# Performance work log

Measured on AMD Instinct MI355X. Metric: run time of the kernel, lower is better.

The kernel has to match this reference:

```python
import jax, jax.numpy as jnp
import numpy as np

H = 2048      # hidden_size
I = 8192      # dense intermediate_size
MI = 1024     # moe_intermediate_size
E = 8         # num_local_experts
K = 2         # num_experts_per_tok
B, S = 2, 1024
EPS = 1e-6
ROOT = H ** (-0.5)


def _rms(x, w=None, eps=EPS):
    # fp32 RMSNorm matching _Gemma4CPURMSNorm; w=None -> no-scale variant
    ms = jnp.mean(x * x, axis=-1, keepdims=True) + eps
    y = x * jax.lax.rsqrt(ms)
    return y * w if w is not None else y


def _gelu_tanh(x):
    # gelu_pytorch_tanh == tanh-approximate gelu
    return jax.nn.gelu(x, approximate=True)


def setup_inputs() -> dict:
    key = jax.random.key(0)
    ks = jax.random.split(key, 10)
    s = 0.02
    return {
        "hidden_states": jax.random.normal(ks[0], (B, S, H), jnp.float32),
        # RMSNorm scales (init ones, as in nn.Parameter(torch.ones(dim)))
        "rn_pre1": jnp.ones((H,), jnp.float32),
        "rn_pre2": jnp.ones((H,), jnp.float32),
        "rn_post1": jnp.ones((H,), jnp.float32),
        "rn_post2": jnp.ones((H,), jnp.float32),
        "rn_post": jnp.ones((H,), jnp.float32),
        # dense GLU MLP weights, stored (in, out)
        "w_gate": jax.random.normal(ks[1], (H, I), jnp.float32) * s,
        "w_up":   jax.random.normal(ks[2], (H, I), jnp.float32) * s,
        "w_down": jax.random.normal(ks[3], (I, H), jnp.float32) * s,
        # router
        "router_w": jax.random.normal(ks[4], (H, E), jnp.float32) * s,
        "router_scale": jnp.ones((H,), jnp.float32),
        "per_expert_scale": jnp.ones((E,), jnp.float32),
        # per-expert GLU weights, stacked over experts
        "we_gate": jax.random.normal(ks[5], (E, H, MI), jnp.float32) * s,
        "we_up":   jax.random.normal(ks[6], (E, H, MI), jnp.float32) * s,
        "we_down": jax.random.normal(ks[7], (E, MI, H), jnp.float32) * s,
    }


def reference(hidden_states, rn_pre1, rn_pre2, rn_post1, rn_post2, rn_post,
              w_gate, w_up, w_down, router_w, router_scale, per_expert_scale,
              we_gate, we_up, we_down):
    b, s, h = hidden_states.shape
    T = b * s

    # --- dense branch ---
    dense_in = _rms(hidden_states, rn_pre1)                      # (B,S,H)
    dense_out = (_gelu_tanh(dense_in @ w_gate) * (dense_in @ w_up)) @ w_down
    dense_out = _rms(dense_out, rn_post1)                        # (B,S,H)

    # --- router (takes the raw residual, applies its own no-scale RMSNorm) ---
    x = hidden_states.reshape(T, h)
    xr = _rms(x) * router_scale * ROOT                           # (T,H)
    router_logits = xr @ router_w                                # (T,E)
    probs = jax.nn.softmax(router_logits, axis=-1)
    top_w, top_i = jax.lax.top_k(probs, K)                       # (T,K)
    top_w = top_w / jnp.sum(top_w, axis=-1, keepdims=True)
    top_w = top_w * per_expert_scale[top_i]
    aff = jnp.zeros((T, E), x.dtype).at[jnp.arange(T)[:, None], top_i].set(top_w)

    # --- MoE experts (compute all experts, combine with sparse affinities) ---
    moe_in = _rms(hidden_states, rn_pre2).reshape(T, h)          # (T,H)
    g = jnp.einsum('th,ehm->tem', moe_in, we_gate)               # (T,E,MI)
    u = jnp.einsum('th,ehm->tem', moe_in, we_up)
    eo = jnp.einsum('tem,emh->teh', _gelu_tanh(g) * u, we_down)  # (T,E,H)
    moe_out = jnp.einsum('te,teh->th', aff, eo).reshape(b, s, h)
    moe_out = _rms(moe_out, rn_post2)

    return _rms(dense_out + moe_out, rn_post)
```

## Files before the change

kernel.cpp:

```cpp
#include <hip/hip_runtime.h>
#include <stdint.h>

#define TOK 2048
#define HD  2048
#define ID  8192
#define MID 1024
#define NE  8
#define KSPLIT 4

typedef __attribute__((ext_vector_type(8))) short s16x8;
typedef __attribute__((ext_vector_type(4))) short s16x4;
typedef __attribute__((ext_vector_type(4))) float f32x4;

constexpr float EPSF  = 1e-6f;
constexpr float ROOTF = 0.02209708691207961f;

#define MFMA(a, b, c) __builtin_amdgcn_mfma_f32_16x16x32_bf16(a, b, c, 0, 0, 0)

__device__ __forceinline__ void gload16(const void* g, void* l) {
  __builtin_amdgcn_global_load_lds(
      (const __attribute__((address_space(1))) void*)g,
      (__attribute__((address_space(3))) void*)l, 16, 0, 0);
}

__device__ __forceinline__ short f2bf(float f) {
  union { float f; uint32_t u; } v; v.f = f;
  uint32_t r = v.u + 0x7fffu + ((v.u >> 16) & 1u);
  return (short)(r >> 16);
}

__device__ __forceinline__ float gelu_tanh(float x) {
  float x3 = x * x * x;
  float u = 0.7978845608028654f * (x + 0.044715f * x3);
  return 0.5f * x * (1.0f + tanhf(u));
}

__global__ __launch_bounds__(256) void k_rms_router(
    const float* __restrict__ x, const float* __restrict__ rnp1,
    const float* __restrict__ rnp2, const float* __restrict__ rsc,
    const float* __restrict__ rw, const float* __restrict__ pes,
    short* __restrict__ rms1, short* __restrict__ rms2,
    int* __restrict__ cnt, int* __restrict__ tokl,
    float* __restrict__ wgtl, int* __restrict__ slotl) {
  const int t = blockIdx.x, tid = threadIdx.x;
  const size_t base = (size_t)t * HD;
  f32x4 v[2];
  float ss = 0.f;
#pragma unroll
  for (int i = 0; i < 2; ++i) {
    v[i] = *(const f32x4*)(x + base + tid * 4 + i * 1024);
#pragma unroll
    for (int j = 0; j < 4; ++j) ss += v[i][j] * v[i][j];
  }
  __shared__ float sr[4];
  __shared__ float sl[32];
#pragma unroll
  for (int off = 32; off; off >>= 1) ss += __shfl_down(ss, off, 64);
  if ((tid & 63) == 0) sr[tid >> 6] = ss;
  __syncthreads();
  const float inv = rsqrtf((sr[0] + sr[1] + sr[2] + sr[3]) * (1.0f / HD) + EPSF);
  float p[8] = {0, 0, 0, 0, 0, 0, 0, 0};
#pragma unroll
  for (int i = 0; i < 2; ++i) {
    const int h = tid * 4 + i * 1024;
    f32x4 w1 = *(const f32x4*)(rnp1 + h);
    f32x4 w2 = *(const f32x4*)(rnp2 + h);
    f32x4 sc = *(const f32x4*)(rsc + h);
    s16x4 o1, o2;
#pragma unroll
    for (int j = 0; j < 4; ++j) {
      float xn = v[i][j] * inv;
      o1[j] = f2bf(xn * w1[j]);
      o2[j] = f2bf(xn * w2[j]);
      float xq = xn * sc[j] * ROOTF;
      const float* rr = rw + (size_t)(h + j) * NE;
      f32x4 ra = *(const f32x4*)rr;
      f32x4 rb = *(const f32x4*)(rr + 4);
      p[0] += xq * ra[0]; p[1] += xq * ra[1]; p[2] += xq * ra[2]; p[3] += xq * ra[3];
      p[4] += xq * rb[0]; p[5] += xq * rb[1]; p[6] += xq * rb[2]; p[7] += xq * rb[3];
    }
    *(s16x4*)(rms1 + base + h) = o1;
    *(s16x4*)(rms2 + base + h) = o2;
  }
#pragma unroll
  for (int e = 0; e < 8; ++e)
#pragma unroll
    for (int off = 32; off; off >>= 1) p[e] += __shfl_down(p[e], off, 64);
  if ((tid & 63) == 0) {
#pragma unroll
    for (int e = 0; e < 8; ++e) sl[(tid >> 6) * 8 + e] = p[e];
  }
  __syncthreads();
  if (tid == 0) {
    float l[8];
#pragma unroll
    for (int e = 0; e < 8; ++e) l[e] = sl[e] + sl[8 + e] + sl[16 + e] + sl[24 + e];
    int i1 = 0;
#pragma unroll
    for (int e = 1; e < 8; ++e) if (l[e] > l[i1]) i1 = e;
    int i2 = (i1 == 0) ? 1 : 0;
#pragma unroll
    for (int e = 0; e < 8; ++e) if (e != i1 && l[e] > l[i2]) i2 = e;
    float p2 = expf(l[i2] - l[i1]);
    float s = 1.0f + p2;
    float w1 = (1.0f / s) * pes[i1];
    float w2 = (p2 / s) * pes[i2];
    int q1 = atomicAdd(&cnt[i1], 1);
    tokl[i1 * TOK + q1] = t; wgtl[i1 * TOK + q1] = w1; slotl[i1 * TOK + q1] = 0;
    int q2 = atomicAdd(&cnt[i2], 1);
    tokl[i2 * TOK + q2] = t; wgtl[i2 * TOK + q2] = w2; slotl[i2 * TOK + q2] = 1;
  }
}

__global__ __launch_bounds__(256) void k_transpose(
    const float* __restrict__ in, short* __restrict__ out, int R, int C) {
  __shared__ float tile[64 * 65];
  const int tid = threadIdx.x;
  const int c0 = blockIdx.x * 64, r0 = blockIdx.y * 64;
  const size_t bo = (size_t)blockIdx.z * R * C;
#pragma unroll
  for (int i = 0; i < 4; ++i) {
    int idx = tid + 256 * i;
    int r = idx >> 4, c4 = idx & 15;
    f32x4 f = *(const f32x4*)(in + bo + (size_t)(r0 + r) * C + c0 + c4 * 4);
#pragma unroll
    for (int j = 0; j < 4; ++j) tile[(c4 * 4 + j) * 65 + r] = f[j];
  }
  __syncthreads();
#pragma unroll
  for (int i = 0; i < 2; ++i) {
    int ch = tid + 256 * i;
    int c = ch >> 3, rs = ch & 7;
    s16x8 o;
#pragma unroll
    for (int q = 0; q < 8; ++q) o[q] = f2bf(tile[c * 65 + rs * 8 + q]);
    *(s16x8*)(out + bo + (size_t)(c0 + c) * R + r0 + rs * 8) = o;
  }
}

__global__ __launch_bounds__(256) void k_dense_gateup(
    const short* __restrict__ wgT, const short* __restrict__ wuT,
    const short* __restrict__ xin,
    short* __restrict__ act) {
  __shared__ short sW[128 * 32];
  __shared__ short sX[128 * 32];
  const int tid = threadIdx.x;
  const int n0 = blockIdx.x * 64, t0 = blockIdx.y * 128;
  const int lane = tid & 63, wave = tid >> 6;
  const int ln15 = lane & 15, k8 = (lane >> 4) * 8;
  const int nsub = (wave & 1) * 32, tsub = (wave >> 1) * 64;
  const int srow = tid >> 2, skc = (tid & 3) * 8;
  const short* gW0 = wgT + (size_t)(n0 + srow) * HD + skc;
  const short* gW1 = wuT + (size_t)(n0 + srow) * HD + skc;
  const short* gX0 = xin + (size_t)(t0 + srow) * HD + skc;
  const short* gX1 = xin + (size_t)(t0 + 64 + srow) * HD + skc;
  char* lW = (char*)sW + wave * 1024;
  char* lX = (char*)sX + wave * 1024;
  f32x4 accg[2][4], accu[2][4];
#pragma unroll
  for (int m = 0; m < 2; ++m)
#pragma unroll
    for (int n = 0; n < 4; ++n) { accg[m][n] = (f32x4)0.f; accu[m][n] = (f32x4)0.f; }
  for (int kt = 0; kt < HD / 32; ++kt) {
    const int ko = kt * 32;
    __syncthreads();
    gload16(gW0 + ko, lW);
    gload16(gW1 + ko, lW + 4096);
    gload16(gX0 + ko, lX);
    gload16(gX1 + ko, lX + 4096);
    __syncthreads();
    s16x8 ag[2], au[2], bx[4];
#pragma unroll
    for (int m = 0; m < 2; ++m) {
      ag[m] = *(const s16x8*)(sW + (nsub + m * 16 + ln15) * 32 + k8);
      au[m] = *(const s16x8*)(sW + (64 + nsub + m * 16 + ln15) * 32 + k8);
    }
#pragma unroll
    for (int n = 0; n < 4; ++n)
      bx[n] = *(const s16x8*)(sX + (tsub + n * 16 + ln15) * 32 + k8);
#pragma unroll
    for (int m = 0; m < 2; ++m)
#pragma unroll
      for (int n = 0; n < 4; ++n) {
        accg[m][n] = MFMA(ag[m], bx[n], accg[m][n]);
        accu[m][n] = MFMA(au[m], bx[n], accu[m][n]);
      }
  }
#pragma unroll
  for (int m = 0; m < 2; ++m)
#pragma unroll
    for (int n = 0; n < 4; ++n) {
      const int t = t0 + tsub + n * 16 + ln15;
      const int ib = n0 + nsub + m * 16 + (lane >> 4) * 4;
      s16x4 o;
#pragma unroll
      for (int r = 0; r < 4; ++r)
        o[r] = f2bf(gelu_tanh(accg[m][n][r]) * accu[m][n][r]);
      *(s16x4*)(act + (size_t)t * ID + ib) = o;
    }
}

__global__ __launch_bounds__(256) void k_dense_down(
    const short* __restrict__ wdT,
    const short* __restrict__ act,
    float* __restrict__ dparts) {
  __shared__ short sW[128 * 32];
  __shared__ short sX[128 * 32];
  const int tid = threadIdx.x;
  const int n0 = blockIdx.x * 128, t0 = blockIdx.y * 128;
  const int kbase = blockIdx.z * (ID / KSPLIT);
  const int lane = tid & 63, wave = tid >> 6;
  const int wr = wave >> 1, wc = wave & 1;
  const int ln15 = lane & 15, k8 = (lane >> 4) * 8;
  const int srow = tid >> 2, skc = (tid & 3) * 8;
  const short* gW0 = wdT + (size_t)(n0 + srow) * ID + kbase + skc;
  const short* gW1 = wdT + (size_t)(n0 + 64 + srow) * ID + kbase + skc;
  const short* gX0 = act + (size_t)(t0 + srow) * ID + kbase + skc;
  const short* gX1 = act + (size_t)(t0 + 64 + srow) * ID + kbase + skc;
  char* lW = (char*)sW + wave * 1024;
  char* lX = (char*)sX + wave * 1024;
  f32x4 acc[4][4];
#pragma unroll
  for (int m = 0; m < 4; ++m)
#pragma unroll
    for (int n = 0; n < 4; ++n) acc[m][n] = (f32x4)0.f;
  for (int kt = 0; kt < ID / KSPLIT / 32; ++kt) {
    const int ko = kt * 32;
    __syncthreads();
    gload16(gW0 + ko, lW);
    gload16(gW1 + ko, lW + 4096);
    gload16(gX0 + ko, lX);
    gload16(gX1 + ko, lX + 4096);
    __syncthreads();
    s16x8 a[4], b[4];
#pragma unroll
    for (int m = 0; m < 4; ++m)
      a[m] = *(const s16x8*)(sW + (wr * 64 + m * 16 + ln15) * 32 + k8);
#pragma unroll
    for (int n = 0; n < 4; ++n)
      b[n] = *(const s16x8*)(sX + (wc * 64 + n * 16 + ln15) * 32 + k8);
#pragma unroll
    for (int m = 0; m < 4; ++m)
#pragma unroll
      for (int n = 0; n < 4; ++n) acc[m][n] = MFMA(a[m], b[n], acc[m][n]);
  }
  float* dst = dparts + (size_t)blockIdx.z * TOK * HD;
#pragma unroll
  for (int n = 0; n < 4; ++n) {
    const int t = t0 + wc * 64 + n * 16 + ln15;
#pragma unroll
    for (int m = 0; m < 4; ++m) {
      const int h = n0 + wr * 64 + m * 16 + (lane >> 4) * 4;
      *(f32x4*)(dst + (size_t)t * HD + h) = acc[m][n];
    }
  }
}

__global__ __launch_bounds__(256) void k_exp_gateup(
    const short* __restrict__ wegT, const short* __restrict__ weuT,
    const short* __restrict__ rms2,
    const int* __restrict__ cnt, const int* __restrict__ tokl,
    short* __restrict__ acte) {
  const int e = blockIdx.z;
  const int cn = cnt[e];
  const int t0 = blockIdx.y * 128;
  if (t0 >= cn) return;
  const int n0 = blockIdx.x * 64;
  __shared__ short sW[128 * 32];
  __shared__ short sX[128 * 32];
  const int tid = threadIdx.x;
  const int lane = tid & 63, wave = tid >> 6;
  const int ln15 = lane & 15, k8 = (lane >> 4) * 8;
  const int nsub = (wave & 1) * 32, tsub = (wave >> 1) * 64;
  const int srow = tid >> 2, skc = (tid & 3) * 8;
  const int* tl = tokl + e * TOK;
  int r0 = t0 + srow, r1 = t0 + 64 + srow;
  int tk0 = tl[r0 < cn ? r0 : cn - 1];
  int tk1 = tl[r1 < cn ? r1 : cn - 1];
  const short* gW0 = wegT + (size_t)e * MID * HD + (size_t)(n0 + srow) * HD + skc;
  const short* gW1 = weuT + (size_t)e * MID * HD + (size_t)(n0 + srow) * HD + skc;
  const short* gX0 = rms2 + (size_t)tk0 * HD + skc;
  const short* gX1 = rms2 + (size_t)tk1 * HD + skc;
  char* lW = (char*)sW + wave * 1024;
  char* lX = (char*)sX + wave * 1024;
  f32x4 accg[2][4], accu[2][4];
#pragma unroll
  for (int m = 0; m < 2; ++m)
#pragma unroll
    for (int n = 0; n < 4; ++n) { accg[m][n] = (f32x4)0.f; accu[m][n] = (f32x4)0.f; }
  for (int kt = 0; kt < HD / 32; ++kt) {
    const int ko = kt * 32;
    __syncthreads();
    gload16(gW0 + ko, lW);
    gload16(gW1 + ko, lW + 4096);
    gload16(gX0 + ko, lX);
    gload16(gX1 + ko, lX + 4096);
    __syncthreads();
    s16x8 ag[2], au[2], bx[4];
#pragma unroll
    for (int m = 0; m < 2; ++m) {
      ag[m] = *(const s16x8*)(sW + (nsub + m * 16 + ln15) * 32 + k8);
      au[m] = *(const s16x8*)(sW + (64 + nsub + m * 16 + ln15) * 32 + k8);
    }
#pragma unroll
    for (int n = 0; n < 4; ++n)
      bx[n] = *(const s16x8*)(sX + (tsub + n * 16 + ln15) * 32 + k8);
#pragma unroll
    for (int m = 0; m < 2; ++m)
#pragma unroll
      for (int n = 0; n < 4; ++n) {
        accg[m][n] = MFMA(ag[m], bx[n], accg[m][n]);
        accu[m][n] = MFMA(au[m], bx[n], accu[m][n]);
      }
  }
#pragma unroll
  for (int m = 0; m < 2; ++m)
#pragma unroll
    for (int n = 0; n < 4; ++n) {
      const int r = t0 + tsub + n * 16 + ln15;
      if (r < cn) {
        const int ib = n0 + nsub + m * 16 + (lane >> 4) * 4;
        s16x4 o;
#pragma unroll
        for (int q = 0; q < 4; ++q)
          o[q] = f2bf(gelu_tanh(accg[m][n][q]) * accu[m][n][q]);
        *(s16x4*)(acte + (size_t)e * TOK * MID + (size_t)r * MID + ib) = o;
      }
    }
}

__global__ __launch_bounds__(256) void k_exp_down(
    const short* __restrict__ wedT,
    const short* __restrict__ acte,
    const int* __restrict__ cnt, const int* __restrict__ tokl,
    const float* __restrict__ wgtl, const int* __restrict__ slotl,
    float* __restrict__ moep) {
  const int e = blockIdx.z;
  const int cn = cnt[e];
  const int t0 = blockIdx.y * 128;
  if (t0 >= cn) return;
  const int n0 = blockIdx.x * 128;
  __shared__ short sW[128 * 32];
  __shared__ short sX[128 * 32];
  const int tid = threadIdx.x;
  const int lane = tid & 63, wave = tid >> 6;
  const int wr = wave >> 1, wc = wave & 1;
  const int ln15 = lane & 15, k8 = (lane >> 4) * 8;
  const int srow = tid >> 2, skc = (tid & 3) * 8;
  const short* wb = wedT + (size_t)e * HD * MID;
  const short* gW0 = wb + (size_t)(n0 + srow) * MID + skc;
  const short* gW1 = wb + (size_t)(n0 + 64 + srow) * MID + skc;
  const short* ab = acte + (size_t)e * TOK * MID;
  const short* gX0 = ab + (size_t)(t0 + srow) * MID + skc;
  const short* gX1 = ab + (size_t)(t0 + 64 + srow) * MID + skc;
  char* lW = (char*)sW + wave * 1024;
  char* lX = (char*)sX + wave * 1024;
  f32x4 acc[4][4];
#pragma unroll
  for (int m = 0; m < 4; ++m)
#pragma unroll
    for (int n = 0; n < 4; ++n) acc[m][n] = (f32x4)0.f;
  for (int kt = 0; kt < MID / 32; ++kt) {
    const int ko = kt * 32;
    __syncthreads();
    gload16(gW0 + ko, lW);
    gload16(gW1 + ko, lW + 4096);
    gload16(gX0 + ko, lX);
    gload16(gX1 + ko, lX + 4096);
    __syncthreads();
    s16x8 a[4], b[4];
#pragma unroll
    for (int m = 0; m < 4; ++m)
      a[m] = *(const s16x8*)(sW + (wr * 64 + m * 16 + ln15) * 32 + k8);
#pragma unroll
    for (int n = 0; n < 4; ++n)
      b[n] = *(const s16x8*)(sX + (wc * 64 + n * 16 + ln15) * 32 + k8);
#pragma unroll
    for (int m = 0; m < 4; ++m)
#pragma unroll
      for (int n = 0; n < 4; ++n) acc[m][n] = MFMA(a[m], b[n], acc[m][n]);
  }
#pragma unroll
  for (int n = 0; n < 4; ++n) {
    const int r = t0 + wc * 64 + n * 16 + ln15;
    if (r < cn) {
      const int tk = tokl[e * TOK + r];
      const float wf = wgtl[e * TOK + r];
      const int sl = slotl[e * TOK + r];
      float* dst = moep + (size_t)sl * TOK * HD + (size_t)tk * HD;
#pragma unroll
      for (int m = 0; m < 4; ++m) {
        const int h = n0 + wr * 64 + m * 16 + (lane >> 4) * 4;
        f32x4 v = acc[m][n] * wf;
        *(f32x4*)(dst + h) = v;
      }
    }
  }
}

__global__ __launch_bounds__(256) void k_final(
    const float* __restrict__ dparts, const float* __restrict__ moep,
    const float* __restrict__ rno1, const float* __restrict__ rno2,
    const float* __restrict__ rnof, float* __restrict__ out) {
  const int t = blockIdx.x, tid = threadIdx.x;
  const size_t base = (size_t)t * HD;
  f32x4 dv[2], mv[2];
  float ssd = 0.f, ssm = 0.f;
#pragma unroll
  for (int i = 0; i < 2; ++i) {
    const int h = tid * 4 + i * 1024;
    dv[i] = (f32x4)0.f;
#pragma unroll
    for (int z = 0; z < KSPLIT; ++z)
      dv[i] += *(const f32x4*)(dparts + (size_t)z * TOK * HD + base + h);
    f32x4 a = *(const f32x4*)(moep + base + h);
    f32x4 b = *(const f32x4*)(moep + (size_t)TOK * HD + base + h);
    mv[i] = a + b;
#pragma unroll
    for (int j = 0; j < 4; ++j) { ssd += dv[i][j] * dv[i][j]; ssm += mv[i][j] * mv[i][j]; }
  }
  __shared__ float sr[8];
#pragma unroll
  for (int off = 32; off; off >>= 1) {
    ssd += __shfl_down(ssd, off, 64);
    ssm += __shfl_down(ssm, off, 64);
  }
  if ((tid & 63) == 0) { sr[tid >> 6] = ssd; sr[4 + (tid >> 6)] = ssm; }
  __syncthreads();
  const float invd = rsqrtf((sr[0] + sr[1] + sr[2] + sr[3]) * (1.0f / HD) + EPSF);
  const float invm = rsqrtf((sr[4] + sr[5] + sr[6] + sr[7]) * (1.0f / HD) + EPSF);
  f32x4 y[2];
  float ssy = 0.f;
#pragma unroll
  for (int i = 0; i < 2; ++i) {
    const int h = tid * 4 + i * 1024;
    f32x4 w1 = *(const f32x4*)(rno1 + h);
    f32x4 w2 = *(const f32x4*)(rno2 + h);
#pragma unroll
    for (int j = 0; j < 4; ++j) {
      y[i][j] = dv[i][j] * invd * w1[j] + mv[i][j] * invm * w2[j];
      ssy += y[i][j] * y[i][j];
    }
  }
  __syncthreads();
#pragma unroll
  for (int off = 32; off; off >>= 1) ssy += __shfl_down(ssy, off, 64);
  if ((tid & 63) == 0) sr[tid >> 6] = ssy;
  __syncthreads();
  const float invy = rsqrtf((sr[0] + sr[1] + sr[2] + sr[3]) * (1.0f / HD) + EPSF);
#pragma unroll
  for (int i = 0; i < 2; ++i) {
    const int h = tid * 4 + i * 1024;
    f32x4 w = *(const f32x4*)(rnof + h);
    f32x4 o;
#pragma unroll
    for (int j = 0; j < 4; ++j) o[j] = y[i][j] * invy * w[j];
    *(f32x4*)(out + base + h) = o;
  }
}

extern "C" void kernel_launch(void* const* d_in, const int* in_sizes, int n_in,
                              void* d_out, int out_size, void* d_ws, size_t ws_size,
                              hipStream_t stream) {
  (void)in_sizes; (void)n_in; (void)out_size;
  const float* x    = (const float*)d_in[0];
  const float* rnp1 = (const float*)d_in[1];
  const float* rnp2 = (const float*)d_in[2];
  const float* rno1 = (const float*)d_in[3];
  const float* rno2 = (const float*)d_in[4];
  const float* rnof = (const float*)d_in[5];
  const float* wg   = (const float*)d_in[6];
  const float* wu   = (const float*)d_in[7];
  const float* wd   = (const float*)d_in[8];
  const float* rw   = (const float*)d_in[9];
  const float* rsc  = (const float*)d_in[10];
  const float* pes  = (const float*)d_in[11];
  const float* weg  = (const float*)d_in[12];
  const float* weu  = (const float*)d_in[13];
  const float* wed  = (const float*)d_in[14];
  float* out = (float*)d_out;

  char* ws = (char*)d_ws;
  size_t off = 0;
  auto alloc = [&](size_t bytes) -> void* {
    void* p = ws + off;
    off += (bytes + 255) & ~(size_t)255;
    return p;
  };
  const size_t IH  = (size_t)ID * HD;
  const size_t EMH = (size_t)NE * MID * HD;
  short* wgT   = (short*)alloc(IH * 2);
  short* wuT   = (short*)alloc(IH * 2);
  short* wdT   = (short*)alloc(IH * 2);
  short* wegT  = (short*)alloc(EMH * 2);
  short* weuT  = (short*)alloc(EMH * 2);
  short* wedT  = (short*)alloc(EMH * 2);
  short* rms1  = (short*)alloc((size_t)TOK * HD * 2);
  short* rms2  = (short*)alloc((size_t)TOK * HD * 2);
  short* actb  = (short*)alloc((size_t)TOK * ID * 2);
  short* acte  = (short*)alloc((size_t)NE * TOK * MID * 2);
  float* moep  = (float*)alloc((size_t)2 * TOK * HD * 4);
  int*   cnt   = (int*)alloc(NE * 4);
  int*   tokl  = (int*)alloc((size_t)NE * TOK * 4);
  float* wgtl  = (float*)alloc((size_t)NE * TOK * 4);
  int*   slotl = (int*)alloc((size_t)NE * TOK * 4);
  if (off > ws_size) return;
  float* dparts = (float*)wgT;

  hipMemsetAsync(cnt, 0, NE * 4, stream);
  k_rms_router<<<TOK, 256, 0, stream>>>(x, rnp1, rnp2, rsc, rw, pes,
                                        rms1, rms2, cnt, tokl, wgtl, slotl);
  k_transpose<<<dim3(ID / 64, HD / 64, 1), 256, 0, stream>>>(wg, wgT, HD, ID);
  k_transpose<<<dim3(ID / 64, HD / 64, 1), 256, 0, stream>>>(wu, wuT, HD, ID);
  k_transpose<<<dim3(HD / 64, ID / 64, 1), 256, 0, stream>>>(wd, wdT, ID, HD);
  k_transpose<<<dim3(MID / 64, HD / 64, NE), 256, 0, stream>>>(weg, wegT, HD, MID);
  k_transpose<<<dim3(MID / 64, HD / 64, NE), 256, 0, stream>>>(weu, weuT, HD, MID);
  k_transpose<<<dim3(HD / 64, MID / 64, NE), 256, 0, stream>>>(wed, wedT, MID, HD);
  k_dense_gateup<<<dim3(ID / 64, TOK / 128), 256, 0, stream>>>(wgT, wuT, rms1, actb);
  k_dense_down<<<dim3(HD / 128, TOK / 128, KSPLIT), 256, 0, stream>>>(wdT, actb, dparts);
  k_exp_gateup<<<dim3(MID / 64, TOK / 128, NE), 256, 0, stream>>>(wegT, weuT, rms2,
                                                                  cnt, tokl, acte);
  k_exp_down<<<dim3(HD / 128, TOK / 128, NE), 256, 0, stream>>>(wedT, acte, cnt, tokl,
                                                                wgtl, slotl, moep);
  k_final<<<TOK, 256, 0, stream>>>(dparts, moep, rno1, rno2, rnof, out);
}
```

Measured before the change: 630.9 us.

## Triple-buffer LDS tiles with async prefetch in all four GEMM kernels

Converts the single-buffered LDS staging in the dense and expert GEMM kernels into a three-stage ring. Global-to-LDS loads for tile k+2 are issued while tile k is being consumed, and explicit vmcnt/lgkmcnt waits plus raw barriers replace the two __syncthreads per iteration. The goal is to hide global memory latency behind MFMA work. In exchange LDS use per block triples (48KB), which may lower occupancy, and correctness depends on the manual wait counts matching the number of loads in flight.

```diff
diff --git a/kernel.cpp b/kernel.cpp
--- a/kernel.cpp
+++ b/kernel.cpp
@@ -16,6 +16,11 @@
 constexpr float ROOTF = 0.02209708691207961f;
 
 #define MFMA(a, b, c) __builtin_amdgcn_mfma_f32_16x16x32_bf16(a, b, c, 0, 0, 0)
+
+#define BAR() __builtin_amdgcn_s_barrier()
+#define VMCNT(n) asm volatile("s_waitcnt vmcnt(" #n ")" ::: "memory")
+#define LGKM0() do { asm volatile("s_waitcnt lgkmcnt(0)" ::: "memory"); \
+                     __builtin_amdgcn_sched_barrier(0); } while (0)
 
 __device__ __forceinline__ void gload16(const void* g, void* l) {
   __builtin_amdgcn_global_load_lds(
@@ -142,8 +147,8 @@
     const short* __restrict__ wgT, const short* __restrict__ wuT,
     const short* __restrict__ xin,
     short* __restrict__ act) {
-  __shared__ short sW[128 * 32];
-  __shared__ short sX[128 * 32];
+  __shared__ short sW[3][128 * 32];
+  __shared__ short sX[3][128 * 32];
   const int tid = threadIdx.x;
   const int n0 = blockIdx.x * 64, t0 = blockIdx.y * 128;
   const int lane = tid & 63, wave = tid >> 6;
@@ -154,30 +159,41 @@
   const short* gW1 = wuT + (size_t)(n0 + srow) * HD + skc;
   const short* gX0 = xin + (size_t)(t0 + srow) * HD + skc;
   const short* gX1 = xin + (size_t)(t0 + 64 + srow) * HD + skc;
-  char* lW = (char*)sW + wave * 1024;
-  char* lX = (char*)sX + wave * 1024;
-  f32x4 accg[2][4], accu[2][4];
-#pragma unroll
-  for (int m = 0; m < 2; ++m)
-#pragma unroll
-    for (int n = 0; n < 4; ++n) { accg[m][n] = (f32x4)0.f; accu[m][n] = (f32x4)0.f; }
-  for (int kt = 0; kt < HD / 32; ++kt) {
+  const int NT = HD / 32;
+  auto STAGE = [&](int kt, int b) {
     const int ko = kt * 32;
-    __syncthreads();
+    char* lW = (char*)sW[b] + wave * 1024;
+    char* lX = (char*)sX[b] + wave * 1024;
     gload16(gW0 + ko, lW);
     gload16(gW1 + ko, lW + 4096);
     gload16(gX0 + ko, lX);
     gload16(gX1 + ko, lX + 4096);
-    __syncthreads();
+  };
+  f32x4 accg[2][4], accu[2][4];
+#pragma unroll
+  for (int m = 0; m < 2; ++m)
+#pragma unroll
+    for (int n = 0; n < 4; ++n) { accg[m][n] = (f32x4)0.f; accu[m][n] = (f32x4)0.f; }
+  STAGE(0, 0); STAGE(1, 1);
+  VMCNT(4);
+  BAR();
+  int bc = 0, bs = 2;
+  for (int kt = 0; kt < NT; ++kt) {
+    if (kt + 2 < NT)      { STAGE(kt + 2, bs); VMCNT(8); }
+    else if (kt + 1 < NT) { VMCNT(4); }
+    else                  { VMCNT(0); }
+    BAR();
     s16x8 ag[2], au[2], bx[4];
 #pragma unroll
     for (int m = 0; m < 2; ++m) {
-      ag[m] = *(const s16x8*)(sW + (nsub + m * 16 + ln15) * 32 + k8);
-      au[m] = *(const s16x8*)(sW + (64 + nsub + m * 16 + ln15) * 32 + k8);
+      ag[m] = *(const s16x8*)(sW[bc] + (nsub + m * 16 + ln15) * 32 + k8);
+      au[m] = *(const s16x8*)(sW[bc] + (64 + nsub + m * 16 + ln15) * 32 + k8);
     }
 #pragma unroll
     for (int n = 0; n < 4; ++n)
-      bx[n] = *(const s16x8*)(sX + (tsub + n * 16 + ln15) * 32 + k8);
+      bx[n] = *(const s16x8*)(sX[bc] + (tsub + n * 16 + ln15) * 32 + k8);
+    LGKM0();
+    BAR();
 #pragma unroll
     for (int m = 0; m < 2; ++m)
 #pragma unroll
@@ -185,6 +201,8 @@
         accg[m][n] = MFMA(ag[m], bx[n], accg[m][n]);
         accu[m][n] = MFMA(au[m], bx[n], accu[m][n]);
       }
+    bc = (bc == 2) ? 0 : bc + 1;
+    bs = (bs == 2) ? 0 : bs + 1;
   }
 #pragma unroll
   for (int m = 0; m < 2; ++m)
@@ -204,8 +222,8 @@
     const short* __restrict__ wdT,
     const short* __restrict__ act,
     float* __restrict__ dparts) {
-  __shared__ short sW[128 * 32];
-  __shared__ short sX[128 * 32];
+  __shared__ short sW[3][128 * 32];
+  __shared__ short sX[3][128 * 32];
   const int tid = threadIdx.x;
   const int n0 = blockIdx.x * 128, t0 = blockIdx.y * 128;
   const int kbase = blockIdx.z * (ID / KSPLIT);
@@ -217,32 +235,45 @@
   const short* gW1 = wdT + (size_t)(n0 + 64 + srow) * ID + kbase + skc;
   const short* gX0 = act + (size_t)(t0 + srow) * ID + kbase + skc;
   const short* gX1 = act + (size_t)(t0 + 64 + srow) * ID + kbase + skc;
-  char* lW = (char*)sW + wave * 1024;
-  char* lX = (char*)sX + wave * 1024;
-  f32x4 acc[4][4];
-#pragma unroll
-  for (int m = 0; m < 4; ++m)
-#pragma unroll
-    for (int n = 0; n < 4; ++n) acc[m][n] = (f32x4)0.f;
-  for (int kt = 0; kt < ID / KSPLIT / 32; ++kt) {
+  const int NT = ID / KSPLIT / 32;
+  auto STAGE = [&](int kt, int b) {
     const int ko = kt * 32;
-    __syncthreads();
+    char* lW = (char*)sW[b] + wave * 1024;
+    char* lX = (char*)sX[b] + wave * 1024;
     gload16(gW0 + ko, lW);
     gload16(gW1 + ko, lW + 4096);
     gload16(gX0 + ko, lX);
     gload16(gX1 + ko, lX + 4096);
-    __syncthreads();
+  };
+  f32x4 acc[4][4];
+#pragma unroll
+  for (int m = 0; m < 4; ++m)
+#pragma unroll
+    for (int n = 0; n < 4; ++n) acc[m][n] = (f32x4)0.f;
+  STAGE(0, 0); STAGE(1, 1);
+  VMCNT(4);
+  BAR();
+  int bc = 0, bs = 2;
+  for (int kt = 0; kt < NT; ++kt) {
+    if (kt + 2 < NT)      { STAGE(kt + 2, bs); VMCNT(8); }
+    else if (kt + 1 < NT) { VMCNT(4); }
+    else                  { VMCNT(0); }
+    BAR();
     s16x8 a[4], b[4];
 #pragma unroll
     for (int m = 0; m < 4; ++m)
-      a[m] = *(const s16x8*)(sW + (wr * 64 + m * 16 + ln15) * 32 + k8);
+      a[m] = *(const s16x8*)(sW[bc] + (wr * 64 + m * 16 + ln15) * 32 + k8);
 #pragma unroll
     for (int n = 0; n < 4; ++n)
-      b[n] = *(const s16x8*)(sX + (wc * 64 + n * 16 + ln15) * 32 + k8);
+      b[n] = *(const s16x8*)(sX[bc] + (wc * 64 + n * 16 + ln15) * 32 + k8);
+    LGKM0();
+    BAR();
 #pragma unroll
     for (int m = 0; m < 4; ++m)
 #pragma unroll
       for (int n = 0; n < 4; ++n) acc[m][n] = MFMA(a[m], b[n], acc[m][n]);
+    bc = (bc == 2) ? 0 : bc + 1;
+    bs = (bs == 2) ? 0 : bs + 1;
   }
   float* dst = dparts + (size_t)blockIdx.z * TOK * HD;
 #pragma unroll
@@ -266,8 +297,8 @@
   const int t0 = blockIdx.y * 128;
   if (t0 >= cn) return;
   const int n0 = blockIdx.x * 64;
-  __shared__ short sW[128 * 32];
-  __shared__ short sX[128 * 32];
+  __shared__ short sW[3][128 * 32];
+  __shared__ short sX[3][128 * 32];
   const int tid = threadIdx.x;
   const int lane = tid & 63, wave = tid >> 6;
   const int ln15 = lane & 15, k8 = (lane >> 4) * 8;
@@ -281,30 +312,41 @@
   const short* gW1 = weuT + (size_t)e * MID * HD + (size_t)(n0 + srow) * HD + skc;
   const short* gX0 = rms2 + (size_t)tk0 * HD + skc;
   const short* gX1 = rms2 + (size_t)tk1 * HD + skc;
-  char* lW = (char*)sW + wave * 1024;
-  char* lX = (char*)sX + wave * 1024;
-  f32x4 accg[2][4], accu[2][4];
-#pragma unroll
-  for (int m = 0; m < 2; ++m)
-#pragma unroll
-    for (int n = 0; n < 4; ++n) { accg[m][n] = (f32x4)0.f; accu[m][n] = (f32x4)0.f; }
-  for (int kt = 0; kt < HD / 32; ++kt) {
+  const int NT = HD / 32;
+  auto STAGE = [&](int kt, int b) {
     const int ko = kt * 32;
-    __syncthreads();
+    char* lW = (char*)sW[b] + wave * 1024;
+    char* lX = (char*)sX[b] + wave * 1024;
     gload16(gW0 + ko, lW);
     gload16(gW1 + ko, lW + 4096);
     gload16(gX0 + ko, lX);
     gload16(gX1 + ko, lX + 4096);
-    __syncthreads();
+  };
+  f32x4 accg[2][4], accu[2][4];
+#pragma unroll
+  for (int m = 0; m < 2; ++m)
+#pragma unroll
+    for (int n = 0; n < 4; ++n) { accg[m][n] = (f32x4)0.f; accu[m][n] = (f32x4)0.f; }
+  STAGE(0, 0); STAGE(1, 1);
+  VMCNT(4);
+  BAR();
+  int bc = 0, bs = 2;
+  for (int kt = 0; kt < NT; ++kt) {
+    if (kt + 2 < NT)      { STAGE(kt + 2, bs); VMCNT(8); }
+    else if (kt + 1 < NT) { VMCNT(4); }
+    else                  { VMCNT(0); }
+    BAR();
     s16x8 ag[2], au[2], bx[4];
 #pragma unroll
     for (int m = 0; m < 2; ++m) {
-      ag[m] = *(const s16x8*)(sW + (nsub + m * 16 + ln15) * 32 + k8);
-      au[m] = *(const s16x8*)(sW + (64 + nsub + m * 16 + ln15) * 32 + k8);
+      ag[m] = *(const s16x8*)(sW[bc] + (nsub + m * 16 + ln15) * 32 + k8);
+      au[m] = *(const s16x8*)(sW[bc] + (64 + nsub + m * 16 + ln15) * 32 + k8);
     }
 #pragma unroll
     for (int n = 0; n < 4; ++n)
-      bx[n] = *(const s16x8*)(sX + (tsub + n * 16 + ln15) * 32 + k8);
+      bx[n] = *(const s16x8*)(sX[bc] + (tsub + n * 16 + ln15) * 32 + k8);
+    LGKM0();
+    BAR();
 #pragma unroll
     for (int m = 0; m < 2; ++m)
 #pragma unroll
@@ -312,6 +354,8 @@
         accg[m][n] = MFMA(ag[m], bx[n], accg[m][n]);
         accu[m][n] = MFMA(au[m], bx[n], accu[m][n]);
       }
+    bc = (bc == 2) ? 0 : bc + 1;
+    bs = (bs == 2) ? 0 : bs + 1;
   }
 #pragma unroll
   for (int m = 0; m < 2; ++m)
@@ -340,8 +384,8 @@
   const int t0 = blockIdx.y * 128;
   if (t0 >= cn) return;
   const int n0 = blockIdx.x * 128;
-  __shared__ short sW[128 * 32];
-  __shared__ short sX[128 * 32];
+  __shared__ short sW[3][128 * 32];
+  __shared__ short sX[3][128 * 32];
   const int tid = threadIdx.x;
   const int lane = tid & 63, wave = tid >> 6;
   const int wr = wave >> 1, wc = wave & 1;
@@ -353,32 +397,45 @@
   const short* ab = acte + (size_t)e * TOK * MID;
   const short* gX0 = ab + (size_t)(t0 + srow) * MID + skc;
   const short* gX1 = ab + (size_t)(t0 + 64 + srow) * MID + skc;
-  char* lW = (char*)sW + wave * 1024;
-  char* lX = (char*)sX + wave * 1024;
-  f32x4 acc[4][4];
-#pragma unroll
-  for (int m = 0; m < 4; ++m)
-#pragma unroll
-    for (int n = 0; n < 4; ++n) acc[m][n] = (f32x4)0.f;
-  for (int kt = 0; kt < MID / 32; ++kt) {
+  const int NT = MID / 32;
+  auto STAGE = [&](int kt, int b) {
     const int ko = kt * 32;
-    __syncthreads();
+    char* lW = (char*)sW[b] + wave * 1024;
+    char* lX = (char*)sX[b] + wave * 1024;
     gload16(gW0 + ko, lW);
     gload16(gW1 + ko, lW + 4096);
     gload16(gX0 + ko, lX);
     gload16(gX1 + ko, lX + 4096);
-    __syncthreads();
+  };
+  f32x4 acc[4][4];
+#pragma unroll
+  for (int m = 0; m < 4; ++m)
+#pragma unroll
+    for (int n = 0; n < 4; ++n) acc[m][n] = (f32x4)0.f;
+  STAGE(0, 0); STAGE(1, 1);
+  VMCNT(4);
+  BAR();
+  int bc = 0, bs = 2;
+  for (int kt = 0; kt < NT; ++kt) {
+    if (kt + 2 < NT)      { STAGE(kt + 2, bs); VMCNT(8); }
+    else if (kt + 1 < NT) { VMCNT(4); }
+    else                  { VMCNT(0); }
+    BAR();
     s16x8 a[4], b[4];
 #pragma unroll
     for (int m = 0; m < 4; ++m)
-      a[m] = *(const s16x8*)(sW + (wr * 64 + m * 16 + ln15) * 32 + k8);
+      a[m] = *(const s16x8*)(sW[bc] + (wr * 64 + m * 16 + ln15) * 32 + k8);
 #pragma unroll
     for (int n = 0; n < 4; ++n)
-      b[n] = *(const s16x8*)(sX + (wc * 64 + n * 16 + ln15) * 32 + k8);
+      b[n] = *(const s16x8*)(sX[bc] + (wc * 64 + n * 16 + ln15) * 32 + k8);
+    LGKM0();
+    BAR();
 #pragma unroll
     for (int m = 0; m < 4; ++m)
 #pragma unroll
       for (int n = 0; n < 4; ++n) acc[m][n] = MFMA(a[m], b[n], acc[m][n]);
+    bc = (bc == 2) ? 0 : bc + 1;
+    bs = (bs == 2) ? 0 : bs + 1;
   }
 #pragma unroll
   for (int n = 0; n < 4; ++n) {
```

Measured after the change: 707.1 us. 1.12x slower.

## Replace fused dense gate/up kernel with double-buffered 256x256 GEMMs plus GELU-mul pass

Applied to the files above, without the earlier changes.

Swaps the small 128x64 single-buffered dense gate/up kernel for a 512-thread 256x256-tile bf16 MFMA GEMM. The new GEMM double-buffers LDS via global_load_lds, uses an XOR-swizzled layout and raises wave priority around the MFMAs. It runs once for gate and once for up, writing bf16 intermediates into reused workspace (acte and moep). A separate elementwise kernel then applies gelu(g)*u. The aim is much higher MFMA utilisation and operand reuse, at the cost of about 96 MB of extra HBM traffic for the intermediates, an extra launch, and bf16 rounding of g and u before the GELU.

```diff
diff --git a/kernel.cpp b/kernel.cpp
--- a/kernel.cpp
+++ b/kernel.cpp
@@ -16,6 +16,9 @@
 constexpr float ROOTF = 0.02209708691207961f;
 
 #define MFMA(a, b, c) __builtin_amdgcn_mfma_f32_16x16x32_bf16(a, b, c, 0, 0, 0)
+#define BAR() __builtin_amdgcn_s_barrier()
+#define SCHED0() __builtin_amdgcn_sched_barrier(0)
+#define VMCNT(n) asm volatile("s_waitcnt vmcnt(" #n ")" ::: "memory")
 
 __device__ __forceinline__ void gload16(const void* g, void* l) {
   __builtin_amdgcn_global_load_lds(
@@ -27,6 +30,11 @@
   union { float f; uint32_t u; } v; v.f = f;
   uint32_t r = v.u + 0x7fffu + ((v.u >> 16) & 1u);
   return (short)(r >> 16);
+}
+
+__device__ __forceinline__ float bf2f(short s) {
+  union { uint32_t u; float f; } v; v.u = ((uint32_t)(uint16_t)s) << 16;
+  return v.f;
 }
 
 __device__ __forceinline__ float gelu_tanh(float x) {
@@ -138,66 +146,100 @@
   }
 }
 
-__global__ __launch_bounds__(256) void k_dense_gateup(
-    const short* __restrict__ wgT, const short* __restrict__ wuT,
-    const short* __restrict__ xin,
-    short* __restrict__ act) {
-  __shared__ short sW[128 * 32];
-  __shared__ short sX[128 * 32];
+__global__ __launch_bounds__(512, 2) void k_gemm256(
+    const short* __restrict__ Wt,
+    const short* __restrict__ X,
+    short* __restrict__ C) {
+  __shared__ char lds[2][65536];
   const int tid = threadIdx.x;
-  const int n0 = blockIdx.x * 64, t0 = blockIdx.y * 128;
   const int lane = tid & 63, wave = tid >> 6;
-  const int ln15 = lane & 15, k8 = (lane >> 4) * 8;
-  const int nsub = (wave & 1) * 32, tsub = (wave >> 1) * 64;
-  const int srow = tid >> 2, skc = (tid & 3) * 8;
-  const short* gW0 = wgT + (size_t)(n0 + srow) * HD + skc;
-  const short* gW1 = wuT + (size_t)(n0 + srow) * HD + skc;
-  const short* gX0 = xin + (size_t)(t0 + srow) * HD + skc;
-  const short* gX1 = xin + (size_t)(t0 + 64 + srow) * HD + skc;
-  char* lW = (char*)sW + wave * 1024;
-  char* lX = (char*)sX + wave * 1024;
-  f32x4 accg[2][4], accu[2][4];
-#pragma unroll
-  for (int m = 0; m < 2; ++m)
-#pragma unroll
-    for (int n = 0; n < 4; ++n) { accg[m][n] = (f32x4)0.f; accu[m][n] = (f32x4)0.f; }
-  for (int kt = 0; kt < HD / 32; ++kt) {
-    const int ko = kt * 32;
-    __syncthreads();
-    gload16(gW0 + ko, lW);
-    gload16(gW1 + ko, lW + 4096);
-    gload16(gX0 + ko, lX);
-    gload16(gX1 + ko, lX + 4096);
-    __syncthreads();
-    s16x8 ag[2], au[2], bx[4];
-#pragma unroll
-    for (int m = 0; m < 2; ++m) {
-      ag[m] = *(const s16x8*)(sW + (nsub + m * 16 + ln15) * 32 + k8);
-      au[m] = *(const s16x8*)(sW + (64 + nsub + m * 16 + ln15) * 32 + k8);
-    }
-#pragma unroll
-    for (int n = 0; n < 4; ++n)
-      bx[n] = *(const s16x8*)(sX + (tsub + n * 16 + ln15) * 32 + k8);
-#pragma unroll
-    for (int m = 0; m < 2; ++m)
-#pragma unroll
-      for (int n = 0; n < 4; ++n) {
-        accg[m][n] = MFMA(ag[m], bx[n], accg[m][n]);
-        accu[m][n] = MFMA(au[m], bx[n], accu[m][n]);
+  const int wr = wave >> 2, wc = wave & 3;
+  const int ln15 = lane & 15, l16 = lane >> 4;
+  const int m0 = blockIdx.x * 256, t0 = blockIdx.y * 256;
+  const int swz = (ln15 & 7) << 4;
+  const int srow = tid >> 3;
+  const int sslot = ((tid & 7) ^ ((tid >> 3) & 7)) << 4;
+  const char* Wb = (const char*)Wt;
+  const char* Xb = (const char*)X;
+  auto STAGE = [&](int kt, int s) {
+#pragma unroll
+    for (int c = 0; c < 4; ++c) {
+      gload16(Wb + (size_t)(m0 + c * 64 + srow) * 4096 + kt * 128 + sslot,
+              &lds[s][c * 8192] + wave * 1024);
+      gload16(Xb + (size_t)(t0 + c * 64 + srow) * 4096 + kt * 128 + sslot,
+              &lds[s][32768 + c * 8192] + wave * 1024);
+    }
+  };
+  f32x4 acc[8][4];
+#pragma unroll
+  for (int m = 0; m < 8; ++m)
+#pragma unroll
+    for (int n = 0; n < 4; ++n) acc[m][n] = (f32x4)0.f;
+  const int NT = HD / 64;
+  STAGE(0, 0);
+  STAGE(1, 1);
+  VMCNT(8);
+  SCHED0();
+  BAR();
+#pragma unroll 2
+  for (int kt = 0; kt < NT; ++kt) {
+    const int s = kt & 1;
+    const char* sA = &lds[s][0];
+    const char* sB = &lds[s][32768];
+#pragma unroll
+    for (int mh = 0; mh < 2; ++mh)
+#pragma unroll
+      for (int ks = 0; ks < 2; ++ks) {
+        const int ka = (ks * 64 + l16 * 16) ^ swz;
+        s16x8 a[4], b[4];
+#pragma unroll
+        for (int f = 0; f < 4; ++f)
+          a[f] = *(const s16x8*)(sA + (wr * 128 + mh * 64 + f * 16 + ln15) * 128 + ka);
+#pragma unroll
+        for (int n = 0; n < 4; ++n)
+          b[n] = *(const s16x8*)(sB + (wc * 64 + n * 16 + ln15) * 128 + ka);
+        __builtin_amdgcn_s_setprio(1);
+#pragma unroll
+        for (int f = 0; f < 4; ++f)
+#pragma unroll
+          for (int n = 0; n < 4; ++n)
+            acc[mh * 4 + f][n] = MFMA(a[f], b[n], acc[mh * 4 + f][n]);
+        __builtin_amdgcn_s_setprio(0);
       }
-  }
-#pragma unroll
-  for (int m = 0; m < 2; ++m)
+    BAR();
+    if (kt + 2 < NT) {
+      STAGE(kt + 2, s);
+      VMCNT(8);
+    } else if (kt + 1 < NT) {
+      VMCNT(0);
+    }
+    SCHED0();
+    BAR();
+  }
+#pragma unroll
+  for (int mi = 0; mi < 8; ++mi)
 #pragma unroll
     for (int n = 0; n < 4; ++n) {
-      const int t = t0 + tsub + n * 16 + ln15;
-      const int ib = n0 + nsub + m * 16 + (lane >> 4) * 4;
+      const int t = t0 + wc * 64 + n * 16 + ln15;
+      const int i = m0 + wr * 128 + mi * 16 + l16 * 4;
       s16x4 o;
 #pragma unroll
-      for (int r = 0; r < 4; ++r)
-        o[r] = f2bf(gelu_tanh(accg[m][n][r]) * accu[m][n][r]);
-      *(s16x4*)(act + (size_t)t * ID + ib) = o;
-    }
+      for (int r = 0; r < 4; ++r) o[r] = f2bf(acc[mi][n][r]);
+      *(s16x4*)(C + (size_t)t * ID + i) = o;
+    }
+}
+
+__global__ __launch_bounds__(256) void k_gelumul(
+    const short* __restrict__ g, const short* __restrict__ u,
+    short* __restrict__ o) {
+  const size_t idx = ((size_t)blockIdx.x * 256 + threadIdx.x) * 8;
+  s16x8 gv = *(const s16x8*)(g + idx);
+  s16x8 uv = *(const s16x8*)(u + idx);
+  s16x8 ov;
+#pragma unroll
+  for (int j = 0; j < 8; ++j)
+    ov[j] = f2bf(gelu_tanh(bf2f(gv[j])) * bf2f(uv[j]));
+  *(s16x8*)(o + idx) = ov;
 }
 
 __global__ __launch_bounds__(256) void k_dense_down(
@@ -506,6 +548,8 @@
   int*   slotl = (int*)alloc((size_t)NE * TOK * 4);
   if (off > ws_size) return;
   float* dparts = (float*)wgT;
+  short* gbuf = acte;
+  short* ubuf = (short*)moep;
 
   hipMemsetAsync(cnt, 0, NE * 4, stream);
   k_rms_router<<<TOK, 256, 0, stream>>>(x, rnp1, rnp2, rsc, rw, pes,
@@ -516,7 +560,9 @@
   k_transpose<<<dim3(MID / 64, HD / 64, NE), 256, 0, stream>>>(weg, wegT, HD, MID);
   k_transpose<<<dim3(MID / 64, HD / 64, NE), 256, 0, stream>>>(weu, weuT, HD, MID);
   k_transpose<<<dim3(HD / 64, MID / 64, NE), 256, 0, stream>>>(wed, wedT, MID, HD);
-  k_dense_gateup<<<dim3(ID / 64, TOK / 128), 256, 0, stream>>>(wgT, wuT, rms1, actb);
+  k_gemm256<<<dim3(ID / 256, TOK / 256), 512, 0, stream>>>(wgT, rms1, gbuf);
+  k_gemm256<<<dim3(ID / 256, TOK / 256), 512, 0, stream>>>(wuT, rms1, ubuf);
+  k_gelumul<<<(TOK * (size_t)ID) / (256 * 8), 256, 0, stream>>>(gbuf, ubuf, actb);
   k_dense_down<<<dim3(HD / 128, TOK / 128, KSPLIT), 256, 0, stream>>>(wdT, actb, dparts);
   k_exp_gateup<<<dim3(MID / 64, TOK / 128, NE), 256, 0, stream>>>(wegT, weuT, rms2,
                                                                   cnt, tokl, acte);
```

Measured after the change: 613.7 us. -2.7%, faster.
